# Kernel tuning notes

Hardware: AMD Instinct MI355X
Metric: run time of the kernel (lower is better)

The kernel has to match this reference:

```python
import jax, jax.numpy as jnp
import numpy as np

H = 1024      # hidden_dim
NH = 16       # num_heads
HD = H // NH  # head_dim
FF = 4 * H
EPS = 1e-5

def _ln(x, g, b):
    m = jnp.mean(x, axis=-1, keepdims=True)
    v = jnp.var(x, axis=-1, keepdims=True)
    return (x - m) * jax.lax.rsqrt(v + EPS) * g + b

def setup_inputs() -> dict:
    key = jax.random.key(0)
    ks = jax.random.split(key, 12)
    s = 1.0 / np.sqrt(H)
    inp = {
        'x': jax.random.normal(ks[0], (2, 2048, H), dtype=jnp.float32),
        'Wq': jax.random.normal(ks[1], (H, H), dtype=jnp.float32) * s,
        'bq': jnp.zeros((H,), dtype=jnp.float32),
        'Wk': jax.random.normal(ks[2], (H, H), dtype=jnp.float32) * s,
        'bk': jnp.zeros((H,), dtype=jnp.float32),
        'Wv': jax.random.normal(ks[3], (H, H), dtype=jnp.float32) * s,
        'bv': jnp.zeros((H,), dtype=jnp.float32),
        'Wo': jax.random.normal(ks[4], (H, H), dtype=jnp.float32) * s,
        'bo': jnp.zeros((H,), dtype=jnp.float32),
        'g1': jnp.ones((H,), dtype=jnp.float32),
        'b1': jnp.zeros((H,), dtype=jnp.float32),
        'W1': jax.random.normal(ks[5], (H, FF), dtype=jnp.float32) * s,
        'bf1': jnp.zeros((FF,), dtype=jnp.float32),
        'W2': jax.random.normal(ks[6], (FF, H), dtype=jnp.float32) * (1.0 / np.sqrt(FF)),
        'bf2': jnp.zeros((H,), dtype=jnp.float32),
        'g2': jnp.ones((H,), dtype=jnp.float32),
        'b2': jnp.zeros((H,), dtype=jnp.float32),
    }
    return inp

def reference(x, Wq, bq, Wk, bk, Wv, bv, Wo, bo, g1, b1, W1, bf1, W2, bf2, g2, b2):
    B, S, _ = x.shape
    residual = x
    xn = _ln(x, g1, b1)
    # [B,S,H] -> [B,NH,S,HD]
    def split_heads(t):
        return t.reshape(B, S, NH, HD).transpose(0, 2, 1, 3)
    q = split_heads(xn @ Wq + bq)
    k = split_heads(xn @ Wk + bk)
    v = split_heads(xn @ Wv + bv)
    scores = jnp.einsum('bhqd,bhkd->bhqk', q, k) / np.sqrt(HD).astype(np.float32)
    attn = jax.nn.softmax(scores, axis=-1)
    ctx = jnp.einsum('bhqk,bhkd->bhqd', attn, v)
    ctx = ctx.transpose(0, 2, 1, 3).reshape(B, S, H)
    out = ctx @ Wo + bo + residual
    residual = out
    on = _ln(out, g2, b2)
    out = jax.nn.relu(on @ W1 + bf1) @ W2 + bf2 + residual
    return out
```

## Files before the change

kernel.cpp:

```cpp
#include <hip/hip_runtime.h>
#include <hip/hip_bf16.h>

constexpr int HDIM = 1024;
constexpr int NHEAD = 16;
constexpr int FFDIM = 4096;
constexpr int SEQLEN = 2048;
constexpr int NTOK = 4096;

typedef __bf16 bf16x8 __attribute__((ext_vector_type(8)));
typedef float f32x4 __attribute__((ext_vector_type(4)));
typedef short s16x4 __attribute__((ext_vector_type(4)));

union U16x8 {
    s16x4 h[2];
    bf16x8 v;
    int4 raw;
    unsigned u[4];
    short s[8];
};

__device__ __forceinline__ short f2bf(float f) {
    union { float f; unsigned u; } c;
    c.f = f;
    return (short)((c.u + 0x8000u) >> 16);
}

__device__ __forceinline__ unsigned cvtpk(float a, float b) {
    __hip_bfloat162 h = __float22bfloat162_rn(float2{a, b});
    return *reinterpret_cast<unsigned*>(&h);
}

__device__ __forceinline__ float exp2_raw(float x) {
    float r;
    asm("v_exp_f32 %0, %1" : "=v"(r) : "v"(x));
    return r;
}

__device__ __forceinline__ void gload16(const void* gsrc, void* lds) {
    __builtin_amdgcn_global_load_lds(
        (const __attribute__((address_space(1))) unsigned int*)gsrc,
        (__attribute__((address_space(3))) unsigned int*)lds, 16, 0, 0);
}


constexpr float QSCALE = 0.18033688011112042f;

__global__ __launch_bounds__(256)
void wconv_all(const float* __restrict__ Wq, const float* __restrict__ Wk,
               const float* __restrict__ Wv, const float* __restrict__ Wo,
               const float* __restrict__ W1, const float* __restrict__ W2,
               short* __restrict__ qkvT, short* __restrict__ WoT,
               short* __restrict__ W1T, short* __restrict__ W2T) {
    int i = blockIdx.x;
    const float* W;
    short* WT;
    int K, N, bx, by;
    if (i < 2048) {
        const int w = i >> 9;
        i &= 511;
        K = HDIM; N = HDIM; bx = i & 3; by = i >> 2;
        W = w == 0 ? Wq : w == 1 ? Wk : w == 2 ? Wv : Wo;
        WT = w == 3 ? WoT : qkvT + (size_t)w * HDIM * HDIM;
    } else if (i < 4096) {
        i -= 2048;
        K = HDIM; N = FFDIM; bx = i & 15; by = i >> 4;
        W = W1; WT = W1T;
    } else {
        i -= 4096;
        K = FFDIM; N = HDIM; bx = i & 3; by = i >> 2;
        W = W2; WT = W2T;
    }
    const int n = bx * 256 + threadIdx.x;
    const int g = by >> 2, fc = by & 3;
    const int k0 = g * 32 + fc * 4;
    float a[4], c[4];
#pragma unroll
    for (int j = 0; j < 4; ++j) a[j] = W[(size_t)(k0 + j) * N + n];
#pragma unroll
    for (int j = 0; j < 4; ++j) c[j] = W[(size_t)(k0 + 16 + j) * N + n];
    U16x8 u;
    u.u[0] = cvtpk(a[0], a[1]);
    u.u[1] = cvtpk(a[2], a[3]);
    u.u[2] = cvtpk(c[0], c[1]);
    u.u[3] = cvtpk(c[2], c[3]);
    *(int4*)(WT + (size_t)n * K + by * 8) = u.raw;
}

__global__ __launch_bounds__(256)
void ln_bf16(const float* __restrict__ x, const float* __restrict__ g,
             const float* __restrict__ b, short* __restrict__ out) {
    const int row = blockIdx.x, t = threadIdx.x;
    const float* xr = x + (size_t)row * HDIM;
    float4 v = *(const float4*)&xr[t * 4];
    float s = v.x + v.y + v.z + v.w;
    float ss = v.x * v.x + v.y * v.y + v.z * v.z + v.w * v.w;
#pragma unroll
    for (int o = 32; o > 0; o >>= 1) {
        s += __shfl_down(s, o);
        ss += __shfl_down(ss, o);
    }
    __shared__ float red[8];
    const int wv = t >> 6, ln = t & 63;
    if (ln == 0) { red[wv] = s; red[4 + wv] = ss; }
    __syncthreads();
    s = red[0] + red[1] + red[2] + red[3];
    ss = red[4] + red[5] + red[6] + red[7];
    const float mean = s * (1.0f / HDIM);
    const float var = ss * (1.0f / HDIM) - mean * mean;
    const float rstd = rsqrtf(var + 1e-5f);
    float4 gv = *(const float4*)&g[t * 4];
    float4 bv = *(const float4*)&b[t * 4];
    union { s16x4 h4; uint2 u2; } pk;
    pk.u2.x = cvtpk((v.x - mean) * rstd * gv.x + bv.x, (v.y - mean) * rstd * gv.y + bv.y);
    pk.u2.y = cvtpk((v.z - mean) * rstd * gv.z + bv.z, (v.w - mean) * rstd * gv.w + bv.w);
    const int kk = (t * 4) & 31;
    const int dst = ((t * 4) & ~31) + ((kk & 15) >> 2) * 8 + (kk >> 4) * 4;
    *(s16x4*)&out[(size_t)row * HDIM + dst] = pk.h4;
}

template <int BM, int BN, int MODE>
__global__ __launch_bounds__(256, 4)
void gemm_bf16(const short* __restrict__ A, const short* __restrict__ BT,
               const float* __restrict__ bias, const float* __restrict__ resid,
               void* __restrict__ outp, int M, int N, int K,
               const float* __restrict__ bias2, const float* __restrict__ bias3,
               void* __restrict__ out3) {
    constexpr int MI = BM / 32, NJ = BN / 32;
    constexpr int NSEG = (BM + BN) / 16;
    __shared__ short LdsF[2 * (BM + BN) * 32];
    const int tid = threadIdx.x;
    const int lane = tid & 63, wave = tid >> 6;
    const int wm = wave >> 1, wn = wave & 1;
    const int l15 = lane & 15, lg = lane >> 4;
    const int lsw = lg ^ ((l15 >> 1) & 3);
    const int m0 = blockIdx.x * BM, n0 = blockIdx.y * BN;
    const int nk = K >> 5;
    const int sr = lane >> 2;
    const int sc8 = (((lane & 3) ^ ((sr >> 1) & 3))) * 8;

    auto stage = [&](int buf, int kt) {
#pragma unroll
        for (int p = 0; p < NSEG / 4; ++p) {
            const int s = wave + p * 4;
            const short* src = (s < BM / 16)
                ? A + (size_t)(m0 + s * 16 + sr) * K + kt * 32 + sc8
                : BT + (size_t)(n0 + (s - BM / 16) * 16 + sr) * K + kt * 32 + sc8;
            const int off = __builtin_amdgcn_readfirstlane(buf * (BM + BN) * 64 + s * 1024);
            gload16(src, (char*)LdsF + off);
        }
    };

    f32x4 acc[MI][NJ] = {};
    stage(0, 0);
    for (int kt = 0; kt < nk; ++kt) {
        const int buf = kt & 1;
        __syncthreads();
        if (kt + 1 < nk) stage(buf ^ 1, kt + 1);
        bf16x8 af[MI], bfr[NJ];
#pragma unroll
        for (int i = 0; i < MI; ++i)
            af[i] = *(const bf16x8*)&LdsF[buf * (BM + BN) * 32 +
                                          (wm * (BM / 2) + i * 16 + l15) * 32 + lsw * 8];
#pragma unroll
        for (int j = 0; j < NJ; ++j)
            bfr[j] = *(const bf16x8*)&LdsF[buf * (BM + BN) * 32 +
                                           (BM + wn * (BN / 2) + j * 16 + l15) * 32 + lsw * 8];
#pragma unroll
        for (int i = 0; i < MI; ++i)
#pragma unroll
            for (int j = 0; j < NJ; ++j)
                acc[i][j] = __builtin_amdgcn_mfma_f32_16x16x32_bf16(af[i], bfr[j], acc[i][j], 0, 0, 0);
    }

    const int rbase = m0 + wm * (BM / 2);
    const int cbase = n0 + wn * (BN / 2);
    if constexpr (MODE == 0) {
#pragma unroll
        for (int i = 0; i < MI; ++i)
#pragma unroll
            for (int j = 0; j < NJ; ++j) {
                const int c = cbase + j * 16 + l15;
                const float bv = bias[c];
#pragma unroll
                for (int ii = 0; ii < 4; ++ii) {
                    const int r = rbase + i * 16 + lg * 4 + ii;
                    const size_t idx = (size_t)r * N + c;
                    ((float*)outp)[idx] = acc[i][j][ii] + bv + resid[idx];
                }
            }
    } else if constexpr (MODE == 1) {
#pragma unroll
        for (int i = 0; i < MI; ++i)
#pragma unroll
            for (int j = 0; j < NJ; ++j) {
                const int c = cbase + j * 16 + l15;
                const float bv = bias[c];
                const int cp = (c & ~31) | ((l15 >> 2) * 8 + (j & 1) * 4 + (l15 & 3));
#pragma unroll
                for (int ii = 0; ii < 4; ++ii) {
                    const int r = rbase + i * 16 + lg * 4 + ii;
                    float v = acc[i][j][ii] + bv;
                    v = v > 0.0f ? v : 0.0f;
                    ((short*)outp)[(size_t)r * N + cp] = f2bf(v);
                }
            }
    } else {
        const int which = n0 >> 10;
        if (which < 2) {
            const float* bb = which == 0 ? bias : bias2;
            const float qs = which == 0 ? QSCALE : 1.0f;
            short* QKp = (short*)outp;
#pragma unroll
            for (int i = 0; i < MI; ++i)
#pragma unroll
                for (int j = 0; j < NJ; ++j) {
                    const int c = cbase + j * 16 + l15;
                    const float bv = bb[c & 1023];
                    const int cp = (c & ~31) | ((l15 >> 2) * 8 + (j & 1) * 4 + (l15 & 3));
#pragma unroll
                    for (int ii = 0; ii < 4; ++ii) {
                        const int r = rbase + i * 16 + lg * 4 + ii;
                        QKp[(size_t)r * 2048 + cp] = f2bf((acc[i][j][ii] + bv) * qs);
                    }
                }
        } else {
            short* VTp = (short*)out3;
#pragma unroll
            for (int j = 0; j < NJ; ++j) {
                const int c = cbase + j * 16 + l15;
                const int cc = c - 2048;
                const int hh = cc >> 6, dd = cc & 63;
                const float bv = bias3[cc];
#pragma unroll
                for (int i = 0; i < MI; ++i) {
                    const int r0 = rbase + i * 16 + lg * 4;
                    const int bb_ = r0 >> 11;
                    const int s0 = r0 & (SEQLEN - 1);
                    const int sbase = (s0 & ~31) + lg * 8 + (i & 1) * 4;
                    union { s16x4 h4; uint2 u2; } pk;
                    pk.u2.x = cvtpk(acc[i][j][0] + bv, acc[i][j][1] + bv);
                    pk.u2.y = cvtpk(acc[i][j][2] + bv, acc[i][j][3] + bv);
                    *(s16x4*)&VTp[(((size_t)(bb_ * NHEAD + hh)) * 64 + dd) * SEQLEN + sbase] = pk.h4;
                }
            }
        }
    }
}

__global__ __launch_bounds__(256, 4)
void attn_fwd(const short* __restrict__ QK, const short* __restrict__ VT,
              short* __restrict__ ctx) {
    __shared__ short KlF[2 * 4096];
    __shared__ short VlF[2 * 4096];
    const int tid = threadIdx.x, lane = tid & 63, wave = tid >> 6;
    const int l15 = lane & 15, lg = lane >> 4;
    const int lsw = lg ^ ((l15 >> 1) & 3);
    const int bid = blockIdx.x;
    const int xcd = bid & 7, li = bid >> 3;
    const int bh = xcd * 4 + (li >> 5);
    const int qt = li & 31;
    const int b = bh >> 4, h = bh & 15;
    const size_t tokbase = (size_t)b * SEQLEN;
    const int sr = lane >> 2;
    const int sc8 = (((lane & 3) ^ ((sr >> 1) & 3))) * 8;

    const short* kp = QK + (tokbase + wave * 16 + sr) * 2048 + 1024 + h * 64 + sc8;
    const short* vp = VT + ((size_t)bh * 64 + wave * 16 + sr) * SEQLEN + sc8;

    auto stage = [&](int buf) {
        const int off = __builtin_amdgcn_readfirstlane(buf * 8192 + wave * 1024);
        gload16(kp, (char*)KlF + off);
        gload16(kp + 32, (char*)KlF + off + 4096);
        gload16(vp, (char*)VlF + off);
        gload16(vp + 32, (char*)VlF + off + 4096);
    };

    const short* qp = QK + (tokbase + qt * 64 + wave * 16 + l15) * 2048 + h * 64;
    bf16x8 qf[2];
    qf[0] = *(const bf16x8*)(qp + lg * 8);
    qf[1] = *(const bf16x8*)(qp + 32 + lg * 8);

    U16x8 uo;
#pragma unroll
    for (int j = 0; j < 8; ++j) uo.s[j] = 0x3F80;
    const bf16x8 onesv = uo.v;

    f32x4 o[4] = {};
    f32x4 Lacc = {};
    stage(0);
    for (int kt = 0; kt < SEQLEN / 64; ++kt) {
        const int buf = kt & 1;
        __syncthreads();
        if (kt + 1 < SEQLEN / 64) {
            kp += 64 * 2048;
            vp += 64;
            stage(buf ^ 1);
        }

        f32x4 sc[4];
        __builtin_amdgcn_s_setprio(1);
#pragma unroll
        for (int j = 0; j < 4; ++j) {
            bf16x8 kf0 = *(const bf16x8*)&KlF[buf * 4096 + (j * 16 + l15) * 32 + lsw * 8];
            bf16x8 kf1 = *(const bf16x8*)&KlF[buf * 4096 + 2048 + (j * 16 + l15) * 32 + lsw * 8];
            f32x4 z = {};
            z = __builtin_amdgcn_mfma_f32_16x16x32_bf16(kf0, qf[0], z, 0, 0, 0);
            sc[j] = __builtin_amdgcn_mfma_f32_16x16x32_bf16(kf1, qf[1], z, 0, 0, 0);
        }
        __builtin_amdgcn_s_setprio(0);

        U16x8 u0, u1;
        u0.u[0] = cvtpk(exp2_raw(sc[0][0]), exp2_raw(sc[0][1]));
        u0.u[1] = cvtpk(exp2_raw(sc[0][2]), exp2_raw(sc[0][3]));
        u0.u[2] = cvtpk(exp2_raw(sc[1][0]), exp2_raw(sc[1][1]));
        u0.u[3] = cvtpk(exp2_raw(sc[1][2]), exp2_raw(sc[1][3]));
        u1.u[0] = cvtpk(exp2_raw(sc[2][0]), exp2_raw(sc[2][1]));
        u1.u[1] = cvtpk(exp2_raw(sc[2][2]), exp2_raw(sc[2][3]));
        u1.u[2] = cvtpk(exp2_raw(sc[3][0]), exp2_raw(sc[3][1]));
        u1.u[3] = cvtpk(exp2_raw(sc[3][2]), exp2_raw(sc[3][3]));

        __builtin_amdgcn_s_setprio(1);
#pragma unroll
        for (int ks = 0; ks < 2; ++ks) {
            const bf16x8 pf = ks == 0 ? u0.v : u1.v;
            Lacc = __builtin_amdgcn_mfma_f32_16x16x32_bf16(onesv, pf, Lacc, 0, 0, 0);
#pragma unroll
            for (int fd = 0; fd < 4; ++fd) {
                bf16x8 vf = *(const bf16x8*)&VlF[buf * 4096 + ks * 2048 + (fd * 16 + l15) * 32 + lsw * 8];
                o[fd] = __builtin_amdgcn_mfma_f32_16x16x32_bf16(vf, pf, o[fd], 0, 0, 0);
            }
        }
        __builtin_amdgcn_s_setprio(0);
    }

    const float rl = 1.0f / Lacc[0];
    const int qrow = qt * 64 + wave * 16 + l15;
    short* crow = ctx + (tokbase + qrow) * HDIM + h * 64;
#pragma unroll
    for (int fd = 0; fd < 4; ++fd) {
        s16x4 v4;
#pragma unroll
        for (int ii = 0; ii < 4; ++ii) v4[ii] = f2bf(o[fd][ii] * rl);
        *(s16x4*)(crow + (fd >> 1) * 32 + lg * 8 + (fd & 1) * 4) = v4;
    }
}

extern "C" void kernel_launch(void* const* d_in, const int* in_sizes, int n_in,
                              void* d_out, int out_size, void* d_ws, size_t ws_size,
                              hipStream_t stream) {
    const float* x  = (const float*)d_in[0];
    const float* Wq = (const float*)d_in[1];
    const float* bq = (const float*)d_in[2];
    const float* Wk = (const float*)d_in[3];
    const float* bk = (const float*)d_in[4];
    const float* Wv = (const float*)d_in[5];
    const float* bv = (const float*)d_in[6];
    const float* Wo = (const float*)d_in[7];
    const float* bo = (const float*)d_in[8];
    const float* g1 = (const float*)d_in[9];
    const float* b1 = (const float*)d_in[10];
    const float* W1 = (const float*)d_in[11];
    const float* bf1 = (const float*)d_in[12];
    const float* W2 = (const float*)d_in[13];
    const float* bf2 = (const float*)d_in[14];
    const float* g2 = (const float*)d_in[15];
    const float* b2 = (const float*)d_in[16];

    char* ws = (char*)d_ws;
    const size_t MB = 1024 * 1024;
    short* qkvT = (short*)(ws + 0 * MB);
    short* WoT  = (short*)(ws + 6 * MB);
    short* W1T  = (short*)(ws + 8 * MB);
    short* W2T  = (short*)(ws + 16 * MB);
    short* xn   = (short*)(ws + 24 * MB);
    short* QKb  = (short*)(ws + 32 * MB);
    short* VTb  = (short*)(ws + 48 * MB);
    short* ctx  = (short*)(ws + 56 * MB);
    float* out1 = (float*)(ws + 64 * MB);
    short* h1   = (short*)(ws + 32 * MB);

    wconv_all<<<6144, 256, 0, stream>>>(Wq, Wk, Wv, Wo, W1, W2, qkvT, WoT, W1T, W2T);

    ln_bf16<<<NTOK, 256, 0, stream>>>(x, g1, b1, xn);

    gemm_bf16<128, 128, 2><<<dim3(NTOK / 128, 3072 / 128), 256, 0, stream>>>(
        xn, qkvT, bq, nullptr, QKb, NTOK, 3072, HDIM, bk, bv, VTb);

    attn_fwd<<<1024, 256, 0, stream>>>(QKb, VTb, ctx);

    gemm_bf16<128, 64, 0><<<dim3(NTOK / 128, HDIM / 64), 256, 0, stream>>>(
        ctx, WoT, bo, x, out1, NTOK, HDIM, HDIM, nullptr, nullptr, nullptr);

    ln_bf16<<<NTOK, 256, 0, stream>>>(out1, g2, b2, xn);

    gemm_bf16<128, 128, 1><<<dim3(NTOK / 128, FFDIM / 128), 256, 0, stream>>>(
        xn, W1T, bf1, nullptr, h1, NTOK, FFDIM, HDIM, nullptr, nullptr, nullptr);

    gemm_bf16<128, 64, 0><<<dim3(NTOK / 128, HDIM / 64), 256, 0, stream>>>(
        h1, W2T, bf2, out1, (float*)d_out, NTOK, HDIM, FFDIM, nullptr, nullptr, nullptr);
}
```

Before: 224.8 us.

## Triple-buffer GEMM LDS staging with explicit vmcnt waits

Changes the bf16 GEMM main loop from double to triple buffering in LDS, prefetching two k-tiles ahead. Each iteration waits with an explicit s_waitcnt vmcnt only on the older tile's loads, then issues a raw barrier. This is meant to keep more global-to-LDS traffic in flight and hide memory latency behind the MFMA work. The cost is 1.5x the shared memory per block and lower occupancy for 256-wide tiles, where launch bounds drop to 3 blocks per CU. The hand-written waitcnt counts are fragile if the number of loads per thread changes.

```diff
diff --git a/kernel.cpp b/kernel.cpp
--- a/kernel.cpp
+++ b/kernel.cpp
@@ -34,6 +34,19 @@
     float r;
     asm("v_exp_f32 %0, %1" : "=v"(r) : "v"(x));
     return r;
+}
+
+template <int N>
+__device__ __forceinline__ void wait_vmcnt() {
+    if constexpr (N == 0) asm volatile("s_waitcnt vmcnt(0)" ::: "memory");
+    else if constexpr (N == 3) asm volatile("s_waitcnt vmcnt(3)" ::: "memory");
+    else if constexpr (N == 4) asm volatile("s_waitcnt vmcnt(4)" ::: "memory");
+    else if constexpr (N == 6) asm volatile("s_waitcnt vmcnt(6)" ::: "memory");
+    else static_assert(N == 0, "unsupported vmcnt");
+}
+__device__ __forceinline__ void barrier_fence() {
+    __builtin_amdgcn_s_barrier();
+    asm volatile("" ::: "memory");
 }
 
 __device__ __forceinline__ void gload16(const void* gsrc, void* lds) {
@@ -119,7 +132,7 @@
 }
 
 template <int BM, int BN, int MODE>
-__global__ __launch_bounds__(256, 4)
+__global__ __launch_bounds__(256, ((BM + BN) == 256) ? 3 : 4)
 void gemm_bf16(const short* __restrict__ A, const short* __restrict__ BT,
                const float* __restrict__ bias, const float* __restrict__ resid,
                void* __restrict__ outp, int M, int N, int K,
@@ -127,7 +140,9 @@
                void* __restrict__ out3) {
     constexpr int MI = BM / 32, NJ = BN / 32;
     constexpr int NSEG = (BM + BN) / 16;
-    __shared__ short LdsF[2 * (BM + BN) * 32];
+    constexpr int PW = NSEG / 4;
+    constexpr int BUFS = (BM + BN) * 32;
+    __shared__ short LdsF[3 * BUFS];
     const int tid = threadIdx.x;
     const int lane = tid & 63, wave = tid >> 6;
     const int wm = wave >> 1, wn = wave & 1;
@@ -140,30 +155,33 @@
 
     auto stage = [&](int buf, int kt) {
 #pragma unroll
-        for (int p = 0; p < NSEG / 4; ++p) {
+        for (int p = 0; p < PW; ++p) {
             const int s = wave + p * 4;
             const short* src = (s < BM / 16)
                 ? A + (size_t)(m0 + s * 16 + sr) * K + kt * 32 + sc8
                 : BT + (size_t)(n0 + (s - BM / 16) * 16 + sr) * K + kt * 32 + sc8;
-            const int off = __builtin_amdgcn_readfirstlane(buf * (BM + BN) * 64 + s * 1024);
+            const int off = __builtin_amdgcn_readfirstlane(buf * BUFS * 2 + s * 1024);
             gload16(src, (char*)LdsF + off);
         }
     };
 
     f32x4 acc[MI][NJ] = {};
     stage(0, 0);
+    if (nk > 1) stage(1, 1);
     for (int kt = 0; kt < nk; ++kt) {
-        const int buf = kt & 1;
-        __syncthreads();
-        if (kt + 1 < nk) stage(buf ^ 1, kt + 1);
+        const int buf = kt % 3;
+        if (kt + 1 < nk) wait_vmcnt<PW>();
+        else wait_vmcnt<0>();
+        barrier_fence();
+        if (kt + 2 < nk) stage((kt + 2) % 3, kt + 2);
         bf16x8 af[MI], bfr[NJ];
 #pragma unroll
         for (int i = 0; i < MI; ++i)
-            af[i] = *(const bf16x8*)&LdsF[buf * (BM + BN) * 32 +
+            af[i] = *(const bf16x8*)&LdsF[buf * BUFS +
                                           (wm * (BM / 2) + i * 16 + l15) * 32 + lsw * 8];
 #pragma unroll
         for (int j = 0; j < NJ; ++j)
-            bfr[j] = *(const bf16x8*)&LdsF[buf * (BM + BN) * 32 +
+            bfr[j] = *(const bf16x8*)&LdsF[buf * BUFS +
                                            (BM + wn * (BN / 2) + j * 16 + l15) * 32 + lsw * 8];
 #pragma unroll
         for (int i = 0; i < MI; ++i)
```

After: 229.0 us. About the same (+1.9%).
